# Kernel tuning notes

Hardware: AMD Instinct MI355X
Metric: run time of the kernel (lower is better)

Reference implementation:

```python
import jax, jax.numpy as jnp
import numpy as np

INF = 1000000000000000.0  # 1e15, matches the TF source

B, H, S, D = 4, 16, 1024, 64


def setup_inputs() -> dict:
    key = jax.random.key(0)
    kq, kk, kv, kp = jax.random.split(key, 4)
    q = jax.random.normal(kq, (B, H, S, D), dtype=jnp.float32)
    k = jax.random.normal(kk, (B, H, S, D), dtype=jnp.float32)
    v = jax.random.normal(kv, (B, H, S, D), dtype=jnp.float32)
    # pad_mask: 1 = masked-out key position, broadcast over heads and queries
    pad_mask = jax.random.randint(kp, (B, 1, 1, S), 0, 2, dtype=jnp.int32)
    # look_ahead_mask: 1 above the diagonal (future positions masked)
    look_ahead_mask = jnp.triu(jnp.ones((S, S), dtype=jnp.int32), k=1)[None, None]
    return {"q": q, "k": k, "v": v, "pad_mask": pad_mask,
            "look_ahead_mask": look_ahead_mask}


def reference(q, k, v, pad_mask, look_ahead_mask):
    d_model = jnp.float32(q.shape[3])
    # scores: (B, H, Sq, Sk)
    score_logits = jnp.einsum("bhqd,bhkd->bhqk", q, k) / jnp.sqrt(d_model)
    if pad_mask is not None:
        score_logits = score_logits + pad_mask.astype(jnp.float32) * (-INF)
    if look_ahead_mask is not None:
        score_logits = score_logits + look_ahead_mask.astype(jnp.float32) * (-INF)
    attention_weights = jax.nn.softmax(score_logits, axis=-1)
    context_vector = jnp.einsum("bhqk,bhkd->bhqd", attention_weights, v)
    return (context_vector, attention_weights)
```

## Files before the change

kernel.cpp:

```cpp
#include <hip/hip_runtime.h>
#include <stdint.h>

#define S 1024
#define D 64
#define TQ 16
#define KT 128
#define NKT 8
#define NEG (-1e15f)
#define SCALE 0.125f

#define WB_STRIDE 1048
#define KB_STRIDE 72
#define VT_STRIDE 136
#define QS_STRIDE 72

typedef __bf16 bf16x8 __attribute__((ext_vector_type(8)));
typedef float f32x4 __attribute__((ext_vector_type(4)));
typedef unsigned short ushort_t;

__device__ __forceinline__ unsigned short f2b(float f) {
  union { float f; uint32_t u; } c; c.f = f;
  uint32_t u = c.u;
  return (unsigned short)((u + 0x7fffu + ((u >> 16) & 1u)) >> 16);
}
__device__ __forceinline__ float b2f(uint32_t u) {
  union { uint32_t u; float f; } c; c.u = u << 16;
  return c.f;
}

__device__ __forceinline__ void barrier_lds_only() {
  asm volatile("s_waitcnt lgkmcnt(0)" ::: "memory");
  __builtin_amdgcn_s_barrier();
  __builtin_amdgcn_sched_barrier(0);
}

__global__ __launch_bounds__(256) void prep_k_kernel(
    const float* __restrict__ Kg, ushort_t* __restrict__ Kb)
{
  const size_t idx = ((size_t)blockIdx.x * 256 + threadIdx.x) * 8;
  float4 a = *(const float4*)(Kg + idx);
  float4 b = *(const float4*)(Kg + idx + 4);
  ushort_t tmp[8];
  tmp[0]=f2b(a.x); tmp[1]=f2b(a.y); tmp[2]=f2b(a.z); tmp[3]=f2b(a.w);
  tmp[4]=f2b(b.x); tmp[5]=f2b(b.y); tmp[6]=f2b(b.z); tmp[7]=f2b(b.w);
  *(uint4*)(Kb + idx) = *(const uint4*)tmp;
}

__global__ __launch_bounds__(256) void prep_vt_kernel(
    const float* __restrict__ Vg, ushort_t* __restrict__ Vt)
{
  __shared__ __align__(16) ushort_t lvt[D * QS_STRIDE];
  const int t = threadIdx.x;
  const int bh = blockIdx.x >> 4;
  const int j0 = (blockIdx.x & 15) << 6;

  {
    const int j = t >> 2, sd = (t & 3) << 4;
    const float* src = Vg + ((size_t)bh * S + j0 + j) * D + sd;
#pragma unroll
    for (int c = 0; c < 4; ++c) {
      float4 f = *(const float4*)(src + (c << 2));
      lvt[(sd + (c << 2) + 0) * QS_STRIDE + j] = f2b(f.x);
      lvt[(sd + (c << 2) + 1) * QS_STRIDE + j] = f2b(f.y);
      lvt[(sd + (c << 2) + 2) * QS_STRIDE + j] = f2b(f.z);
      lvt[(sd + (c << 2) + 3) * QS_STRIDE + j] = f2b(f.w);
    }
  }
  __syncthreads();
  {
    const int d = t >> 2, sj = (t & 3) << 4;
    ushort_t tmp[16];
#pragma unroll
    for (int c = 0; c < 4; ++c)
      *(ushort4*)&tmp[c << 2] = *(const ushort4*)&lvt[d * QS_STRIDE + sj + (c << 2)];
    ushort_t* dst = Vt + ((size_t)bh * D + d) * S + j0 + sj;
    *(uint4*)dst = *(const uint4*)&tmp[0];
    *(uint4*)(dst + 8) = *(const uint4*)&tmp[8];
  }
}

__global__ __launch_bounds__(512, 6) void attn_kernel(
    const float* __restrict__ Qg, const ushort_t* __restrict__ Kb,
    const ushort_t* __restrict__ Vtb, const int* __restrict__ PADg,
    float* __restrict__ OCTX, float* __restrict__ OW)
{
  __shared__ __align__(16) ushort_t wb[TQ * WB_STRIDE];
  __shared__ __align__(16) ushort_t ub[KT * KB_STRIDE];

  const int t  = threadIdx.x;
  const int w  = t >> 6;
  const int l  = t & 63;
  const int la = l & 15;
  const int lb = l >> 4;

  const int hwblk = blockIdx.x;
  const int slot  = hwblk >> 3;
  const int bh    = ((hwblk & 7) << 3) + (slot >> 6);
  const int qt    = slot & 63;
  const int qr0   = qt << 4;

  const size_t head = (size_t)bh * S * D;
  const int* pp = PADg + (size_t)(bh >> 4) * S;

  bf16x8 aq0, aq1;
  {
    const float* qrow = Qg + head + (size_t)(qr0 + la) * D + (lb << 3);
    float4 q00 = *(const float4*)(qrow);
    float4 q01 = *(const float4*)(qrow + 4);
    float4 q10 = *(const float4*)(qrow + 32);
    float4 q11 = *(const float4*)(qrow + 36);
    ushort_t a0[8], a1[8];
    a0[0]=f2b(q00.x); a0[1]=f2b(q00.y); a0[2]=f2b(q00.z); a0[3]=f2b(q00.w);
    a0[4]=f2b(q01.x); a0[5]=f2b(q01.y); a0[6]=f2b(q01.z); a0[7]=f2b(q01.w);
    a1[0]=f2b(q10.x); a1[1]=f2b(q10.y); a1[2]=f2b(q10.z); a1[3]=f2b(q10.w);
    a1[4]=f2b(q11.x); a1[5]=f2b(q11.y); a1[6]=f2b(q11.z); a1[7]=f2b(q11.w);
    aq0 = *(const bf16x8*)a0;
    aq1 = *(const bf16x8*)a1;
  }

  {
    const int kr = l >> 2;
    const int ko = (l & 3) << 4;
    const int rowg = (w << 4) + kr;
    const ushort_t* ksrc = Kb + head + (size_t)rowg * D + ko;
    ushort_t* kdst = &ub[rowg * KB_STRIDE + ko];
    const int j0 = w << 4;
    uint4 kra[2], krb[2];
    kra[0] = *(const uint4*)(ksrc);
    krb[0] = *(const uint4*)(ksrc + 8);
    kra[1] = *(const uint4*)(ksrc + (size_t)(KT * D));
    krb[1] = *(const uint4*)(ksrc + (size_t)(KT * D) + 8);
#pragma unroll
    for (int kt = 0; kt < NKT; ++kt) {
      *(uint4*)kdst = kra[kt & 1];
      *(uint4*)(kdst + 8) = krb[kt & 1];
      if (kt + 2 < NKT) {
        const ushort_t* ns = ksrc + (size_t)(kt + 2) * (KT * D);
        kra[kt & 1] = *(const uint4*)(ns);
        krb[kt & 1] = *(const uint4*)(ns + 8);
      }
      f32x4 acc = {0.f, 0.f, 0.f, 0.f};
      bf16x8 b0 = *(const bf16x8*)&ub[(j0 + la) * KB_STRIDE + (lb << 3)];
      acc = __builtin_amdgcn_mfma_f32_16x16x32_bf16(aq0, b0, acc, 0, 0, 0);
      bf16x8 b1 = *(const bf16x8*)&ub[(j0 + la) * KB_STRIDE + 32 + (lb << 3)];
      acc = __builtin_amdgcn_mfma_f32_16x16x32_bf16(aq1, b1, acc, 0, 0, 0);
#pragma unroll
      for (int i = 0; i < 4; ++i)
        wb[((lb << 2) + i) * WB_STRIDE + kt * KT + j0 + la] = f2b(acc[i]);
    }
  }
  barrier_lds_only();

  const int jh = w >> 2;
  const int d0 = (w & 3) << 4;
  const int vr = l >> 2;
  const int vo = (l & 3) << 4;
  const ushort_t* vsrc = Vtb + (size_t)bh * (D * S) + (size_t)(d0 + vr) * S
                        + jh * 64 + vo;
  ushort_t* vdst = &ub[(d0 + vr) * VT_STRIDE + jh * 64 + vo];
  uint4 vra[2], vrb[2];
  vra[0] = *(const uint4*)(vsrc);
  vrb[0] = *(const uint4*)(vsrc + 8);
  vra[1] = *(const uint4*)(vsrc + KT);
  vrb[1] = *(const uint4*)(vsrc + KT + 8);

#pragma unroll
  for (int rr = 0; rr < 2; ++rr) {
    const int r  = (w << 1) + rr;
    const int qr = qr0 + r;
    float lg[16];
    float m = -3.0e38f;
#pragma unroll
    for (int ii = 0; ii < 8; ++ii) {
      const int j = (l << 1) + (ii << 7);
      uint32_t pr = *(const uint32_t*)&wb[r * WB_STRIDE + j];
      int2 pv = *(const int2*)&pp[j];
      float l0 = b2f(pr & 0xffffu) * SCALE + (pv.x ? NEG : 0.0f) + ((j     > qr) ? NEG : 0.0f);
      float l1 = b2f(pr >> 16)     * SCALE + (pv.y ? NEG : 0.0f) + ((j + 1 > qr) ? NEG : 0.0f);
      lg[2 * ii] = l0; lg[2 * ii + 1] = l1;
      m = fmaxf(m, fmaxf(l0, l1));
    }
#pragma unroll
    for (int off = 32; off > 0; off >>= 1) m = fmaxf(m, __shfl_xor(m, off, 64));
    float sum = 0.f;
#pragma unroll
    for (int x = 0; x < 16; ++x) { lg[x] = __expf(lg[x] - m); sum += lg[x]; }
#pragma unroll
    for (int off = 32; off > 0; off >>= 1) sum += __shfl_xor(sum, off, 64);
    const float inv = 1.0f / sum;
    float* orow = OW + (size_t)(bh * S + qr) * S;
#pragma unroll
    for (int ii = 0; ii < 8; ++ii) {
      const int j = (l << 1) + (ii << 7);
      float w0 = lg[2 * ii] * inv, w1 = lg[2 * ii + 1] * inv;
      *(uint32_t*)&wb[r * WB_STRIDE + j] = ((uint32_t)f2b(w1) << 16) | (uint32_t)f2b(w0);
      unsigned long long uw = ((unsigned long long)__float_as_uint(w1) << 32)
                            | (unsigned long long)__float_as_uint(w0);
      __builtin_nontemporal_store(uw, (unsigned long long*)&orow[j]);
    }
  }
  barrier_lds_only();

  f32x4 cacc = {0.f, 0.f, 0.f, 0.f};
  {
#pragma unroll
    for (int kt = 0; kt < NKT; ++kt) {
      *(uint4*)vdst = vra[kt & 1];
      *(uint4*)(vdst + 8) = vrb[kt & 1];
      if (kt + 2 < NKT) {
        const ushort_t* nv = vsrc + (kt + 2) * KT;
        vra[kt & 1] = *(const uint4*)(nv);
        vrb[kt & 1] = *(const uint4*)(nv + 8);
      }
#pragma unroll
      for (int ks = 0; ks < 2; ++ks) {
        const int jt = jh * 64 + ks * 32;
        bf16x8 af = *(const bf16x8*)&wb[la * WB_STRIDE + kt * KT + jt + (lb << 3)];
        bf16x8 bf = *(const bf16x8*)&ub[(d0 + la) * VT_STRIDE + jt + (lb << 3)];
        cacc = __builtin_amdgcn_mfma_f32_16x16x32_bf16(af, bf, cacc, 0, 0, 0);
      }
    }
  }
  barrier_lds_only();

  float* pbuf = (float*)ub;
  if (w >= 4) {
#pragma unroll
    for (int i = 0; i < 4; ++i)
      pbuf[(w - 4) * 320 + ((lb << 2) + i) * 20 + la] = cacc[i];
  }
  barrier_lds_only();
  if (w < 4) {
#pragma unroll
    for (int i = 0; i < 4; ++i) {
      const int qrow = (lb << 2) + i;
      __builtin_nontemporal_store(
          cacc[i] + pbuf[w * 320 + qrow * 20 + la],
          &OCTX[((size_t)(bh * S) + qr0 + qrow) * D + d0 + la]);
    }
  }
}

extern "C" void kernel_launch(void* const* d_in, const int* in_sizes, int n_in,
                              void* d_out, int out_size, void* d_ws, size_t ws_size,
                              hipStream_t stream) {
  const float* q   = (const float*)d_in[0];
  const float* k   = (const float*)d_in[1];
  const float* v   = (const float*)d_in[2];
  const int*   pad = (const int*)d_in[3];
  float* ctx  = (float*)d_out;
  float* wout = (float*)d_out + (size_t)4 * 16 * S * D;

  ushort_t* Kb  = (ushort_t*)d_ws;
  ushort_t* Vtb = (ushort_t*)d_ws + (size_t)4 * 16 * S * D;

  prep_k_kernel <<<dim3(2048), dim3(256), 0, stream>>>(k, Kb);
  prep_vt_kernel<<<dim3(1024), dim3(256), 0, stream>>>(v, Vtb);
  attn_kernel   <<<dim3(4096), dim3(512), 0, stream>>>(q, Kb, Vtb, pad, ctx, wout);
}
```

Measured before the change: 380.3 us.

## Skip fully masked causal key tiles and fold log2e into the scale

The kernel now works out, per query tile, how many 128-key tiles can hold unmasked keys under the causal mask. It skips QK^T, softmax and PV work for the tiles beyond that and writes zeros for those weight entries directly. A block-wide check falls back to all tiles when some row has every causal key padded, which keeps the uniform-softmax behaviour for that case. The scale now includes log2(e) so the softmax can use exp2f, and the check adds two __syncthreads and a scan of the pad mask per block.

```diff
diff --git a/kernel.cpp b/kernel.cpp
--- a/kernel.cpp
+++ b/kernel.cpp
@@ -7,7 +7,7 @@
 #define KT 128
 #define NKT 8
 #define NEG (-1e15f)
-#define SCALE 0.125f
+#define SCALE2 0.180336880f
 
 #define WB_STRIDE 1048
 #define KB_STRIDE 72
@@ -86,6 +86,7 @@
 {
   __shared__ __align__(16) ushort_t wb[TQ * WB_STRIDE];
   __shared__ __align__(16) ushort_t ub[KT * KB_STRIDE];
+  __shared__ int s_allpad;
 
   const int t  = threadIdx.x;
   const int w  = t >> 6;
@@ -98,9 +99,20 @@
   const int bh    = ((hwblk & 7) << 3) + (slot >> 6);
   const int qt    = slot & 63;
   const int qr0   = qt << 4;
+  const int nv0   = (qt >> 3) + 1;
 
   const size_t head = (size_t)bh * S * D;
   const int* pp = PADg + (size_t)(bh >> 4) * S;
+
+  if (t == 0) s_allpad = 1;
+  __syncthreads();
+  {
+    const bool ok0 = (t > qr0) || (pp[t] != 0);
+    const bool ok1 = (t + 512 > qr0) || (pp[t + 512] != 0);
+    if (!(ok0 && ok1)) s_allpad = 0;
+  }
+  __syncthreads();
+  const int nv = __builtin_amdgcn_readfirstlane(s_allpad ? NKT : nv0);
 
   bf16x8 aq0, aq1;
   {
@@ -128,25 +140,29 @@
     uint4 kra[2], krb[2];
     kra[0] = *(const uint4*)(ksrc);
     krb[0] = *(const uint4*)(ksrc + 8);
-    kra[1] = *(const uint4*)(ksrc + (size_t)(KT * D));
-    krb[1] = *(const uint4*)(ksrc + (size_t)(KT * D) + 8);
+    if (nv > 1) {
+      kra[1] = *(const uint4*)(ksrc + (size_t)(KT * D));
+      krb[1] = *(const uint4*)(ksrc + (size_t)(KT * D) + 8);
+    }
 #pragma unroll
     for (int kt = 0; kt < NKT; ++kt) {
-      *(uint4*)kdst = kra[kt & 1];
-      *(uint4*)(kdst + 8) = krb[kt & 1];
-      if (kt + 2 < NKT) {
-        const ushort_t* ns = ksrc + (size_t)(kt + 2) * (KT * D);
-        kra[kt & 1] = *(const uint4*)(ns);
-        krb[kt & 1] = *(const uint4*)(ns + 8);
-      }
-      f32x4 acc = {0.f, 0.f, 0.f, 0.f};
-      bf16x8 b0 = *(const bf16x8*)&ub[(j0 + la) * KB_STRIDE + (lb << 3)];
-      acc = __builtin_amdgcn_mfma_f32_16x16x32_bf16(aq0, b0, acc, 0, 0, 0);
-      bf16x8 b1 = *(const bf16x8*)&ub[(j0 + la) * KB_STRIDE + 32 + (lb << 3)];
-      acc = __builtin_amdgcn_mfma_f32_16x16x32_bf16(aq1, b1, acc, 0, 0, 0);
-#pragma unroll
-      for (int i = 0; i < 4; ++i)
-        wb[((lb << 2) + i) * WB_STRIDE + kt * KT + j0 + la] = f2b(acc[i]);
+      if (kt < nv) {
+        *(uint4*)kdst = kra[kt & 1];
+        *(uint4*)(kdst + 8) = krb[kt & 1];
+        if (kt + 2 < nv) {
+          const ushort_t* ns = ksrc + (size_t)(kt + 2) * (KT * D);
+          kra[kt & 1] = *(const uint4*)(ns);
+          krb[kt & 1] = *(const uint4*)(ns + 8);
+        }
+        f32x4 acc = {0.f, 0.f, 0.f, 0.f};
+        bf16x8 b0 = *(const bf16x8*)&ub[(j0 + la) * KB_STRIDE + (lb << 3)];
+        acc = __builtin_amdgcn_mfma_f32_16x16x32_bf16(aq0, b0, acc, 0, 0, 0);
+        bf16x8 b1 = *(const bf16x8*)&ub[(j0 + la) * KB_STRIDE + 32 + (lb << 3)];
+        acc = __builtin_amdgcn_mfma_f32_16x16x32_bf16(aq1, b1, acc, 0, 0, 0);
+#pragma unroll
+        for (int i = 0; i < 4; ++i)
+          wb[((lb << 2) + i) * WB_STRIDE + kt * KT + j0 + la] = f2b(acc[i]);
+      }
     }
   }
   barrier_lds_only();
@@ -161,8 +177,10 @@
   uint4 vra[2], vrb[2];
   vra[0] = *(const uint4*)(vsrc);
   vrb[0] = *(const uint4*)(vsrc + 8);
-  vra[1] = *(const uint4*)(vsrc + KT);
-  vrb[1] = *(const uint4*)(vsrc + KT + 8);
+  if (nv > 1) {
+    vra[1] = *(const uint4*)(vsrc + KT);
+    vrb[1] = *(const uint4*)(vsrc + KT + 8);
+  }
 
 #pragma unroll
   for (int rr = 0; rr < 2; ++rr) {
@@ -172,19 +190,23 @@
     float m = -3.0e38f;
 #pragma unroll
     for (int ii = 0; ii < 8; ++ii) {
-      const int j = (l << 1) + (ii << 7);
-      uint32_t pr = *(const uint32_t*)&wb[r * WB_STRIDE + j];
-      int2 pv = *(const int2*)&pp[j];
-      float l0 = b2f(pr & 0xffffu) * SCALE + (pv.x ? NEG : 0.0f) + ((j     > qr) ? NEG : 0.0f);
-      float l1 = b2f(pr >> 16)     * SCALE + (pv.y ? NEG : 0.0f) + ((j + 1 > qr) ? NEG : 0.0f);
-      lg[2 * ii] = l0; lg[2 * ii + 1] = l1;
-      m = fmaxf(m, fmaxf(l0, l1));
+      if (ii < nv) {
+        const int j = (l << 1) + (ii << 7);
+        uint32_t pr = *(const uint32_t*)&wb[r * WB_STRIDE + j];
+        int2 pv = *(const int2*)&pp[j];
+        float l0 = b2f(pr & 0xffffu) * SCALE2 + (pv.x ? NEG : 0.0f) + ((j     > qr) ? NEG : 0.0f);
+        float l1 = b2f(pr >> 16)     * SCALE2 + (pv.y ? NEG : 0.0f) + ((j + 1 > qr) ? NEG : 0.0f);
+        lg[2 * ii] = l0; lg[2 * ii + 1] = l1;
+        m = fmaxf(m, fmaxf(l0, l1));
+      }
     }
 #pragma unroll
     for (int off = 32; off > 0; off >>= 1) m = fmaxf(m, __shfl_xor(m, off, 64));
     float sum = 0.f;
 #pragma unroll
-    for (int x = 0; x < 16; ++x) { lg[x] = __expf(lg[x] - m); sum += lg[x]; }
+    for (int x = 0; x < 16; ++x) {
+      if ((x >> 1) < nv) { lg[x] = exp2f(lg[x] - m); sum += lg[x]; }
+    }
 #pragma unroll
     for (int off = 32; off > 0; off >>= 1) sum += __shfl_xor(sum, off, 64);
     const float inv = 1.0f / sum;
@@ -192,11 +214,15 @@
 #pragma unroll
     for (int ii = 0; ii < 8; ++ii) {
       const int j = (l << 1) + (ii << 7);
-      float w0 = lg[2 * ii] * inv, w1 = lg[2 * ii + 1] * inv;
-      *(uint32_t*)&wb[r * WB_STRIDE + j] = ((uint32_t)f2b(w1) << 16) | (uint32_t)f2b(w0);
-      unsigned long long uw = ((unsigned long long)__float_as_uint(w1) << 32)
-                            | (unsigned long long)__float_as_uint(w0);
-      __builtin_nontemporal_store(uw, (unsigned long long*)&orow[j]);
+      if (ii < nv) {
+        float w0 = lg[2 * ii] * inv, w1 = lg[2 * ii + 1] * inv;
+        *(uint32_t*)&wb[r * WB_STRIDE + j] = ((uint32_t)f2b(w1) << 16) | (uint32_t)f2b(w0);
+        unsigned long long uw = ((unsigned long long)__float_as_uint(w1) << 32)
+                              | (unsigned long long)__float_as_uint(w0);
+        __builtin_nontemporal_store(uw, (unsigned long long*)&orow[j]);
+      } else {
+        __builtin_nontemporal_store(0ull, (unsigned long long*)&orow[j]);
+      }
     }
   }
   barrier_lds_only();
@@ -205,19 +231,21 @@
   {
 #pragma unroll
     for (int kt = 0; kt < NKT; ++kt) {
-      *(uint4*)vdst = vra[kt & 1];
-      *(uint4*)(vdst + 8) = vrb[kt & 1];
-      if (kt + 2 < NKT) {
-        const ushort_t* nv = vsrc + (kt + 2) * KT;
-        vra[kt & 1] = *(const uint4*)(nv);
-        vrb[kt & 1] = *(const uint4*)(nv + 8);
-      }
-#pragma unroll
-      for (int ks = 0; ks < 2; ++ks) {
-        const int jt = jh * 64 + ks * 32;
-        bf16x8 af = *(const bf16x8*)&wb[la * WB_STRIDE + kt * KT + jt + (lb << 3)];
-        bf16x8 bf = *(const bf16x8*)&ub[(d0 + la) * VT_STRIDE + jt + (lb << 3)];
-        cacc = __builtin_amdgcn_mfma_f32_16x16x32_bf16(af, bf, cacc, 0, 0, 0);
+      if (kt < nv) {
+        *(uint4*)vdst = vra[kt & 1];
+        *(uint4*)(vdst + 8) = vrb[kt & 1];
+        if (kt + 2 < nv) {
+          const ushort_t* nvp = vsrc + (kt + 2) * KT;
+          vra[kt & 1] = *(const uint4*)(nvp);
+          vrb[kt & 1] = *(const uint4*)(nvp + 8);
+        }
+#pragma unroll
+        for (int ks = 0; ks < 2; ++ks) {
+          const int jt = jh * 64 + ks * 32;
+          bf16x8 af = *(const bf16x8*)&wb[la * WB_STRIDE + kt * KT + jt + (lb << 3)];
+          bf16x8 bf = *(const bf16x8*)&ub[(d0 + la) * VT_STRIDE + jt + (lb << 3)];
+          cacc = __builtin_amdgcn_mfma_f32_16x16x32_bf16(af, bf, cacc, 0, 0, 0);
+        }
       }
     }
   }
```

Result: slower. 570.7 us (+50.1%).
